# Performance work log

Hardware: AMD Instinct MI355X
Metric: run time of the kernel (lower is better)

Reference implementation:

```python
import jax, jax.numpy as jnp
import numpy as np

K = 8192        # nodes (radio links)
DEG = 32        # out-degree per node
E = K * DEG
GE = 8          # graph_embedding_size
VAR = np.float32((10.0 ** (-19.9) * 5e6) / 10.0)  # output_noise_power / tx_power


def _init_mlp(key, dims_list):
    # per-node stacked Linear params, torch default init U(-1/sqrt(fan_in), 1/sqrt(fan_in))
    params = []
    for (din, dout) in dims_list:
        key, k1, k2 = jax.random.split(key, 3)
        b = float(1.0 / np.sqrt(din))
        params.append(jax.random.uniform(k1, (K, din, dout), minval=-b, maxval=b, dtype=jnp.float32))
        params.append(jax.random.uniform(k2, (K, dout), minval=-b, maxval=b, dtype=jnp.float32))
    return params


def setup_inputs() -> dict:
    key = jax.random.key(0)
    k = jax.random.split(key, 8)
    # edges sorted by src, exactly DEG distinct non-self out-neighbors per node
    src = jnp.repeat(jnp.arange(K), DEG)
    gaps = jax.random.randint(k[0], (K, DEG), 1, (K - 1) // DEG + 1)
    dst = ((jnp.arange(K)[:, None] + jnp.cumsum(gaps, axis=1)) % K).reshape(-1)
    edge_index = jnp.stack([src, dst])
    x = jax.random.uniform(k[1], (K, 1 + GE), dtype=jnp.float32)
    edge_attr = jax.random.uniform(k[2], (E, 1), dtype=jnp.float32)
    H = jax.random.uniform(k[3], (K, K), dtype=jnp.float32) * 1e-12  # |h_ij|^2 gains
    Wm1, bm1, Wm2, bm2 = _init_mlp(k[4], [(2 + GE, 32), (32, 32)])
    Wu1, bu1, Wu2, bu2 = _init_mlp(k[5], [(33 + GE, 16), (16, GE)])
    Wh1, bh1, Wh2, bh2 = _init_mlp(k[6], [(GE, 16), (16, 1)])
    return dict(x=x, edge_attr=edge_attr, H=H, edge_index=edge_index,
                Wm1=Wm1, bm1=bm1, Wm2=Wm2, bm2=bm2,
                Wu1=Wu1, bu1=bu1, Wu2=Wu2, bu2=bu2,
                Wh1=Wh1, bh1=bh1, Wh2=Wh2, bh2=bh2)


def reference(x, edge_attr, H, edge_index,
              Wm1, bm1, Wm2, bm2, Wu1, bu1, Wu2, bu2, Wh1, bh1, Wh2, bh2):
    src, dst = edge_index[0], edge_index[1]

    def conv(x):
        # message: tmp_e = [x[src_e], edge_attr_e]; node src's private mlp_m.
        # edges are contiguous groups of DEG per src -> grouped GEMM as batched einsum
        tmp = jnp.concatenate([x[src], edge_attr], axis=1).reshape(K, DEG, 2 + GE)
        h = jax.nn.relu(jnp.einsum('ked,kdh->keh', tmp, Wm1) + bm1[:, None])
        msg = jax.nn.relu(jnp.einsum('ked,kdh->keh', h, Wm2) + bm2[:, None])
        aggr = msg.sum(axis=1)                                  # [K,32] sum-aggregate
        t = jnp.concatenate([x, aggr], axis=1)                  # [K,41]
        u = jax.nn.relu(jnp.einsum('kd,kdh->kh', t, Wu1) + bu1)
        comb = jax.nn.relu(jnp.einsum('kd,kdh->kh', u, Wu2) + bu2)  # [K,8]
        return jnp.concatenate([x[:, :1], comb], axis=1)        # keep direct-channel col

    x3 = conv(conv(conv(x)))                                    # 3 rounds of LocalConv
    emb = x3[:, 1:]                                             # [K,8]
    hh = jax.nn.relu(jnp.einsum('kd,kdh->kh', emb, Wh1) + bh1)
    p = jax.nn.sigmoid(jnp.einsum('kd,kdh->kh', hh, Wh2) + bh2)[:, 0]  # power in (0,1)

    # per-node (negative) local rate over 1-hop out-neighborhood
    valid = p * jnp.diagonal(H)                                 # p_i * |h_ii|^2
    interf = jax.ops.segment_sum(p[dst] * H[src, dst], src, num_segments=K) + VAR
    interf = jax.lax.stop_gradient(interf)                      # .detach() in original
    local_rate = -jnp.log2(1.0 + valid / interf)                # [K]
    return local_rate
```

## Files before the change

### kernel.cpp

```cpp
#include <hip/hip_runtime.h>
#include <hip/hip_bf16.h>
#include <math.h>

#define KN 8192
#define DEG 32
#define EE (KN*DEG)

#define VAR_F 6.294627058970831e-15f

typedef __attribute__((ext_vector_type(8)))  short bf16x8;
typedef __attribute__((ext_vector_type(16))) float f32x16;

static __device__ __forceinline__ short bf_hi(float f) {
    __hip_bfloat16 h = __float2bfloat16(f);
    return __builtin_bit_cast(short, h);
}
static __device__ __forceinline__ float bf_f(short s) {
    __hip_bfloat16 h = __builtin_bit_cast(__hip_bfloat16, s);
    return __bfloat162float(h);
}

__global__ __launch_bounds__(64, 4) void mpnn_fused(
    const float* __restrict__ x,
    const float* __restrict__ edge_attr,
    const float* __restrict__ Wm1, const float* __restrict__ bm1,
    const float* __restrict__ Wm2, const float* __restrict__ bm2,
    const float* __restrict__ Wu1, const float* __restrict__ bu1,
    const float* __restrict__ Wu2, const float* __restrict__ bu2,
    const float* __restrict__ Wh1, const float* __restrict__ bh1,
    const float* __restrict__ Wh2, const float* __restrict__ bh2,
    float* __restrict__ p_out)
{
    __shared__ __align__(16) float c_lds[32];
    __shared__ float xt[44];
    __shared__ float ubuf[16];

    const int lane = threadIdx.x;
    const int col  = lane & 31;
    const int g    = lane >> 5;
    const int k    = blockIdx.x;

    const int m  = lane & 15;
    const int dg = lane >> 4;
    const int o  = lane & 7;
    const int mg = lane >> 3;

    const float a_e = edge_attr[k*32 + col];

    float wm1[9];
    #pragma unroll
    for (int d = 0; d < 9; ++d) wm1[d] = Wm1[(size_t)k*320 + d*32 + col];

    float w9v[16];
    {
        const float* w9p = Wm1 + (size_t)k*320 + 288;
        float4 wa = *(const float4*)(w9p + g*8);
        float4 wb = *(const float4*)(w9p + g*8 + 4);
        float4 wc = *(const float4*)(w9p + 16 + g*8);
        float4 wd = *(const float4*)(w9p + 16 + g*8 + 4);
        w9v[0]=wa.x;  w9v[1]=wa.y;  w9v[2]=wa.z;  w9v[3]=wa.w;
        w9v[4]=wb.x;  w9v[5]=wb.y;  w9v[6]=wb.z;  w9v[7]=wb.w;
        w9v[8]=wc.x;  w9v[9]=wc.y;  w9v[10]=wc.z; w9v[11]=wc.w;
        w9v[12]=wd.x; w9v[13]=wd.y; w9v[14]=wd.z; w9v[15]=wd.w;
    }

    float wm2f[16];
    #pragma unroll
    for (int s = 0; s < 2; ++s)
        #pragma unroll
        for (int i = 0; i < 8; ++i)
            wm2f[s*8+i] = Wm2[(size_t)k*1024 + (s*16 + g*8 + i)*32 + col];

    const float bm1_i = bm1[k*32 + col];
    const float bm2_i = bm2[k*32 + col];

    float wu1[11];
    #pragma unroll
    for (int t = 0; t < 11; ++t) {
        int d = dg*11 + t;
        wu1[t] = (d < 41) ? Wu1[(size_t)k*656 + d*16 + m] : 0.f;
    }
    const float bu1_m = bu1[k*16 + m];

    const float wu2a  = Wu2[(size_t)k*128 + (mg*2+0)*8 + o];
    const float wu2b  = Wu2[(size_t)k*128 + (mg*2+1)*8 + o];
    const float bu2_o = bu2[k*8 + o];

    float wh1[8];
    #pragma unroll
    for (int d = 0; d < 8; ++d) wh1[d] = Wh1[(size_t)k*128 + d*16 + m];
    const float bh1_m = bh1[k*16 + m];
    const float wh2_m = Wh2[k*16 + m];
    const float bh2_k = bh2[k];

    if (lane < 9) xt[lane] = x[(size_t)k*9 + lane];

    bf16x8 Bhi[2], Blo[2];
    #pragma unroll
    for (int s = 0; s < 2; ++s) {
        #pragma unroll
        for (int i = 0; i < 8; ++i) {
            float wv = wm2f[s*8+i];
            short h = bf_hi(wv);
            Bhi[s][i] = h;
            Blo[s][i] = bf_hi(wv - bf_f(h));
        }
    }

    for (int it = 0; it < 3; ++it) {
        float c = bm1_i;
        #pragma unroll
        for (int d = 0; d < 9; ++d) c = fmaf(xt[d], wm1[d], c);
        if (g == 0) c_lds[col] = c;

        const float4* cb = (const float4*)c_lds;
        float4 q0 = cb[g*2 + 0];
        float4 q1 = cb[g*2 + 1];
        float4 q2 = cb[4 + g*2 + 0];
        float4 q3 = cb[4 + g*2 + 1];
        float cv[16] = {q0.x,q0.y,q0.z,q0.w, q1.x,q1.y,q1.z,q1.w,
                        q2.x,q2.y,q2.z,q2.w, q3.x,q3.y,q3.z,q3.w};
        bf16x8 Ahi[2], Alo[2];
        #pragma unroll
        for (int s = 0; s < 2; ++s) {
            #pragma unroll
            for (int i = 0; i < 8; ++i) {
                int t = s*8 + i;
                float hv = fmaxf(fmaf(a_e, w9v[t], cv[t]), 0.f);
                short h = bf_hi(hv);
                Ahi[s][i] = h;
                Alo[s][i] = bf_hi(hv - bf_f(h));
            }
        }

        f32x16 acc;
        #pragma unroll
        for (int r = 0; r < 16; ++r) acc[r] = 0.f;
        #pragma unroll
        for (int s = 0; s < 2; ++s) {
            acc = __builtin_amdgcn_mfma_f32_32x32x16_bf16(Ahi[s], Bhi[s], acc, 0, 0, 0);
            acc = __builtin_amdgcn_mfma_f32_32x32x16_bf16(Ahi[s], Blo[s], acc, 0, 0, 0);
            acc = __builtin_amdgcn_mfma_f32_32x32x16_bf16(Alo[s], Bhi[s], acc, 0, 0, 0);
        }

        float ag = 0.f;
        #pragma unroll
        for (int r = 0; r < 16; ++r) ag += fmaxf(acc[r] + bm2_i, 0.f);
        ag += __shfl_xor(ag, 32);
        if (g == 0) xt[9 + col] = ag;

        float up = 0.f;
        #pragma unroll
        for (int t = 0; t < 11; ++t) {
            int d = dg*11 + t;
            if (d < 41) up = fmaf(xt[d], wu1[t], up);
        }
        up += __shfl_xor(up, 16);
        up += __shfl_xor(up, 32);
        float u = fmaxf(up + bu1_m, 0.f);
        if (lane < 16) ubuf[lane] = u;

        float cp = wu2a * ubuf[mg*2] + wu2b * ubuf[mg*2 + 1];
        cp += __shfl_xor(cp, 8);
        cp += __shfl_xor(cp, 16);
        cp += __shfl_xor(cp, 32);
        float comb = fmaxf(cp + bu2_o, 0.f);
        if (lane < 8) xt[1 + lane] = comb;
    }

    float hp = 0.f;
    #pragma unroll
    for (int d = 0; d < 8; ++d) hp = fmaf(xt[1 + d], wh1[d], hp);
    float hh = fmaxf(hp + bh1_m, 0.f);
    float pp = hh * wh2_m;
    pp += __shfl_xor(pp, 1);
    pp += __shfl_xor(pp, 2);
    pp += __shfl_xor(pp, 4);
    pp += __shfl_xor(pp, 8);
    float z = pp + bh2_k;
    float p = 1.f / (1.f + expf(-z));
    if (lane == 0) p_out[k] = p;
}

__global__ __launch_bounds__(256) void mpnn_interf(
    const float* __restrict__ H,
    const int* __restrict__ edge_index,
    const float* __restrict__ p,
    float* __restrict__ out)
{
    const int t = blockIdx.x * 256 + threadIdx.x;
    const int s = t >> 5;
    const int e = t & 31;
    const int* dst = edge_index + EE;
    const int d = dst[s*DEG + e];
    float part = p[d] * H[(size_t)s*KN + d];
    part += __shfl_xor(part, 1);
    part += __shfl_xor(part, 2);
    part += __shfl_xor(part, 4);
    part += __shfl_xor(part, 8);
    part += __shfl_xor(part, 16);
    if (e == 0) {
        float interf = part + VAR_F;
        float valid  = p[s] * H[(size_t)s*KN + s];
        out[s] = -log1pf(valid / interf) * 1.4426950408889634f;
    }
}

extern "C" void kernel_launch(void* const* d_in, const int* in_sizes, int n_in,
                              void* d_out, int out_size, void* d_ws, size_t ws_size,
                              hipStream_t stream) {
    const float* x         = (const float*)d_in[0];
    const float* edge_attr = (const float*)d_in[1];
    const float* H         = (const float*)d_in[2];
    const int*   edge_idx  = (const int*)  d_in[3];
    const float* Wm1 = (const float*)d_in[4];
    const float* bm1 = (const float*)d_in[5];
    const float* Wm2 = (const float*)d_in[6];
    const float* bm2 = (const float*)d_in[7];
    const float* Wu1 = (const float*)d_in[8];
    const float* bu1 = (const float*)d_in[9];
    const float* Wu2 = (const float*)d_in[10];
    const float* bu2 = (const float*)d_in[11];
    const float* Wh1 = (const float*)d_in[12];
    const float* bh1 = (const float*)d_in[13];
    const float* Wh2 = (const float*)d_in[14];
    const float* bh2 = (const float*)d_in[15];
    float* out = (float*)d_out;
    float* p_ws = (float*)d_ws;

    mpnn_fused<<<KN, 64, 0, stream>>>(x, edge_attr, Wm1, bm1, Wm2, bm2,
                                      Wu1, bu1, Wu2, bu2, Wh1, bh1, Wh2, bh2,
                                      p_ws);
    mpnn_interf<<<(KN*DEG)/256, 256, 0, stream>>>(H, edge_idx, p_ws, out);
}
```

Measured before the change: 31.98 us.

## Prefetch H gathers in the fused MLP kernel to hide latency

Moves the scattered H[src,dst] and diagonal H loads into the first kernel, where their latency can overlap the MLP compute, and stores the gathered values in a compact workspace. The second kernel then reads contiguous hv_ws and precomputed valid values instead of doing random 8192-stride gathers from H. The cost is extra workspace writes and reads plus more register pressure and memory traffic in the fused kernel.

```diff
diff --git a/kernel.cpp b/kernel.cpp
--- a/kernel.cpp
+++ b/kernel.cpp
@@ -23,13 +23,16 @@
 __global__ __launch_bounds__(64, 4) void mpnn_fused(
     const float* __restrict__ x,
     const float* __restrict__ edge_attr,
+    const float* __restrict__ H,
+    const int* __restrict__ edge_index,
     const float* __restrict__ Wm1, const float* __restrict__ bm1,
     const float* __restrict__ Wm2, const float* __restrict__ bm2,
     const float* __restrict__ Wu1, const float* __restrict__ bu1,
     const float* __restrict__ Wu2, const float* __restrict__ bu2,
     const float* __restrict__ Wh1, const float* __restrict__ bh1,
     const float* __restrict__ Wh2, const float* __restrict__ bh2,
-    float* __restrict__ p_out)
+    float* __restrict__ p_ws, float* __restrict__ valid_ws,
+    float* __restrict__ hv_ws)
 {
     __shared__ __align__(16) float c_lds[32];
     __shared__ float xt[44];
@@ -44,6 +47,11 @@
     const int dg = lane >> 4;
     const int o  = lane & 7;
     const int mg = lane >> 3;
+
+    const int* dst = edge_index + EE;
+    const int dv = dst[k*DEG + col];
+    const float Hv    = H[(size_t)k*KN + dv];
+    const float Hdiag = H[(size_t)k*KN + k];
 
     const float a_e = edge_attr[k*32 + col];
 
@@ -95,6 +103,8 @@
 
     if (lane < 9) xt[lane] = x[(size_t)k*9 + lane];
 
+    if (g == 0) hv_ws[k*DEG + col] = Hv;
+
     bf16x8 Bhi[2], Blo[2];
     #pragma unroll
     for (int s = 0; s < 2; ++s) {
@@ -179,13 +189,17 @@
     pp += __shfl_xor(pp, 8);
     float z = pp + bh2_k;
     float p = 1.f / (1.f + expf(-z));
-    if (lane == 0) p_out[k] = p;
+    if (lane == 0) {
+        p_ws[k] = p;
+        valid_ws[k] = p * Hdiag;
+    }
 }
 
 __global__ __launch_bounds__(256) void mpnn_interf(
-    const float* __restrict__ H,
     const int* __restrict__ edge_index,
-    const float* __restrict__ p,
+    const float* __restrict__ p_ws,
+    const float* __restrict__ valid_ws,
+    const float* __restrict__ hv_ws,
     float* __restrict__ out)
 {
     const int t = blockIdx.x * 256 + threadIdx.x;
@@ -193,7 +207,7 @@
     const int e = t & 31;
     const int* dst = edge_index + EE;
     const int d = dst[s*DEG + e];
-    float part = p[d] * H[(size_t)s*KN + d];
+    float part = p_ws[d] * hv_ws[s*DEG + e];
     part += __shfl_xor(part, 1);
     part += __shfl_xor(part, 2);
     part += __shfl_xor(part, 4);
@@ -201,8 +215,7 @@
     part += __shfl_xor(part, 16);
     if (e == 0) {
         float interf = part + VAR_F;
-        float valid  = p[s] * H[(size_t)s*KN + s];
-        out[s] = -log1pf(valid / interf) * 1.4426950408889634f;
+        out[s] = -log1pf(valid_ws[s] / interf) * 1.4426950408889634f;
     }
 }
 
@@ -226,10 +239,15 @@
     const float* Wh2 = (const float*)d_in[14];
     const float* bh2 = (const float*)d_in[15];
     float* out = (float*)d_out;
-    float* p_ws = (float*)d_ws;
-
-    mpnn_fused<<<KN, 64, 0, stream>>>(x, edge_attr, Wm1, bm1, Wm2, bm2,
+
+    float* p_ws     = (float*)d_ws;
+    float* valid_ws = p_ws + KN;
+    float* hv_ws    = valid_ws + KN;
+
+    mpnn_fused<<<KN, 64, 0, stream>>>(x, edge_attr, H, edge_idx,
+                                      Wm1, bm1, Wm2, bm2,
                                       Wu1, bu1, Wu2, bu2, Wh1, bh1, Wh2, bh2,
-                                      p_ws);
-    mpnn_interf<<<(KN*DEG)/256, 256, 0, stream>>>(H, edge_idx, p_ws, out);
-}
+                                      p_ws, valid_ws, hv_ws);
+    mpnn_interf<<<(KN*DEG)/256, 256, 0, stream>>>(edge_idx, p_ws, valid_ws,
+                                                  hv_ws, out);
+}
```

Measured after the change: 30.97 us. -3.2%, faster.
